# Optimization experiments

Measured on AMD Instinct MI355X. Metric: run time of the kernel, lower is better.

## Reference

```python
import jax, jax.numpy as jnp
import numpy as np

N = 50000          # num nodes
E = 800000         # num edges
DIN = 128          # in_channels
C = 64             # out_channels per head
H = 2              # heads
ED = 32            # edge_dim


def setup_inputs() -> dict:
    key = jax.random.key(0)
    ks = jax.random.split(key, 12)
    s = 1.0 / np.sqrt(DIN)
    se = 1.0 / np.sqrt(ED)
    return {
        "x": jax.random.normal(ks[0], (N, DIN), dtype=jnp.float32),
        "edge_index": jax.random.randint(ks[1], (2, E), 0, N, dtype=jnp.int32),
        "edge_attr": jax.random.normal(ks[2], (E, ED), dtype=jnp.float32),
        "Wq": jax.random.uniform(ks[3], (DIN, H * C), jnp.float32, -s, s),
        "bq": jax.random.uniform(ks[4], (H * C,), jnp.float32, -s, s),
        "Wk": jax.random.uniform(ks[5], (DIN, H * C), jnp.float32, -s, s),
        "bk": jax.random.uniform(ks[6], (H * C,), jnp.float32, -s, s),
        "Wv": jax.random.uniform(ks[7], (DIN, H * C), jnp.float32, -s, s),
        "bv": jax.random.uniform(ks[8], (H * C,), jnp.float32, -s, s),
        "We": jax.random.uniform(ks[9], (ED, H * C), jnp.float32, -se, se),
        "Wskip": jax.random.uniform(ks[10], (DIN, H * C), jnp.float32, -s, s),
        "bskip": jax.random.uniform(ks[11], (H * C,), jnp.float32, -s, s),
    }


def reference(x, edge_index, edge_attr, Wq, bq, Wk, bk, Wv, bv, We, Wskip, bskip):
    src, dst = edge_index[0], edge_index[1]
    # node-level projections [N, H, C]
    q = (x @ Wq + bq).reshape(N, H, C)
    k = (x @ Wk + bk).reshape(N, H, C)
    v = (x @ Wv + bv).reshape(N, H, C)
    e = (edge_attr @ We).reshape(E, H, C)  # lin_edge, no bias

    # per-edge gather
    q_e = q[dst]              # [E, H, C]
    k_e = k[src] + e          # key gets edge features
    alpha = jnp.einsum("ehc,ehc->eh", q_e, k_e) / jnp.sqrt(jnp.float32(C))

    # segment softmax over incoming edges of each dst node
    m = jax.ops.segment_max(alpha, dst, num_segments=N)       # [N, H]
    alpha = jnp.exp(alpha - m[dst])
    denom = jax.ops.segment_sum(alpha, dst, num_segments=N)   # [N, H]
    alpha = alpha / (denom[dst] + 1e-16)

    # weighted aggregation of values (value also gets edge features)
    msg = (v[src] + e) * alpha[..., None]                     # [E, H, C]
    out = jax.ops.segment_sum(msg, dst, num_segments=N)       # [N, H, C]
    out = out.reshape(N, H * C)

    # root weight skip connection (concat=True, beta=False)
    return out + x @ Wskip + bskip
```

## Files before the change

kernel.cpp:

```cpp
#include <hip/hip_runtime.h>
#include <cstdint>

#define NN 50000
#define EE 800000
#define DINC 128
#define HC 128
#define EDC 32
#define CAP 56
#define TILES 1563
#define SCAT_BLKS 3125
#define NB_SCAN 196
#define PREW_GRID (145 + NB_SCAN)

typedef __attribute__((ext_vector_type(8))) short short8;
typedef __attribute__((ext_vector_type(4))) float floatx4;

__device__ __forceinline__ unsigned int pk2(float a, float b){
  unsigned int ua = __float_as_uint(a), ub = __float_as_uint(b);
  ua = (ua + 0x7FFFu + ((ua >> 16) & 1u)) >> 16;
  ub = (ub + 0x7FFFu + ((ub >> 16) & 1u)) & 0xFFFF0000u;
  return ua | ub;
}
__device__ __forceinline__ float bflo(unsigned int p){ return __uint_as_float(p << 16); }
__device__ __forceinline__ float bfhi(unsigned int p){ return __uint_as_float(p & 0xFFFF0000u); }

__device__ __forceinline__ float red32(float r){
  r += __int_as_float(__builtin_amdgcn_update_dpp(0, __float_as_int(r), 0xB1, 0xF, 0xF, true));
  r += __int_as_float(__builtin_amdgcn_update_dpp(0, __float_as_int(r), 0x4E, 0xF, 0xF, true));
  r += __int_as_float(__builtin_amdgcn_update_dpp(0, __float_as_int(r), 0x141, 0xF, 0xF, true));
  r += __int_as_float(__builtin_amdgcn_update_dpp(0, __float_as_int(r), 0x140, 0xF, 0xF, true));
  r += __shfl_xor(r, 16, 32);
  return r;
}

__global__ __launch_bounds__(256) void k_prew(
    const float* __restrict__ Wq, const float* __restrict__ Wk,
    const float* __restrict__ Wv, const float* __restrict__ Wsk,
    const float* __restrict__ We, const float* __restrict__ bq,
    unsigned int* __restrict__ Wp, unsigned int* __restrict__ Wp5,
    float* __restrict__ Pb, int* __restrict__ cnt)
{
  const int b = blockIdx.x, tid = threadIdx.x;
  if (b < 128){
    int idx = b*256 + tid;
    int mat = idx >> 13;
    int r   = idx & 8191;
    int kp  = r >> 7;
    int n   = r & 127;
    const float* W = (mat==0)?Wq:(mat==1)?Wk:(mat==2)?Wv:Wsk;
    Wp[(mat<<13) + n*64 + kp] = pk2(W[(2*kp)*HC + n], W[(2*kp+1)*HC + n]);
  } else if (b < 144){
    if (!Wp5) return;
    int t = (b-128)*256 + tid;
    int kp = t >> 6, n = t & 63;
    int h = n >> 5, j = n & 31;
    const float* wq0 = Wq + (2*kp)*HC + h*64;
    const float* wq1 = wq0 + HC;
    const float* wer = We + j*HC + h*64;
    float d0 = 0.f, d1 = 0.f;
    #pragma unroll 8
    for (int c = 0; c < 64; ++c){
      float w = wer[c];
      d0 += wq0[c]*w; d1 += wq1[c]*w;
    }
    Wp5[n*64 + kp] = pk2(d0, d1);
  } else if (b == 144){
    if (!Wp5 || tid >= 64) return;
    int n = tid, h = n >> 5, j = n & 31;
    const float* wer = We + j*HC + h*64;
    const float* bqh = bq + h*64;
    float s = 0.f;
    #pragma unroll 8
    for (int c = 0; c < 64; ++c) s += bqh[c]*wer[c];
    Pb[n] = s;
  } else {
    int idx = (b-145)*256 + tid;
    if (idx < NN) cnt[idx] = 0;
  }
}

__global__ __launch_bounds__(256) void k_fused(
    const float* __restrict__ x, const unsigned int* __restrict__ Wp,
    const unsigned int* __restrict__ Wp5, const float* __restrict__ Pb,
    const float* __restrict__ bq, const float* __restrict__ bk,
    const float* __restrict__ bv, const float* __restrict__ bsk,
    const int* __restrict__ ei,
    unsigned int* __restrict__ qbf, unsigned int* __restrict__ kvb,
    float* __restrict__ out, float* __restrict__ Pfl,
    int* __restrict__ cnt, int* __restrict__ eidl,
    const int do_scatter)
{
  __shared__ unsigned int sx[32*68];

  if (do_scatter && blockIdx.x >= TILES){
    int e = (blockIdx.x - TILES)*256 + threadIdx.x;
    if (e < EE){
      int d = ei[EE + e];
      int pos = atomicAdd(cnt + d, 1);
      if (pos < CAP) eidl[d*CAP + pos] = e;
    }
    return;
  }

  const int tid = threadIdx.x;
  const int bm  = blockIdx.x * 32;

  for (int idx = tid; idx < 32*32; idx += 256){
    int row = idx >> 5, kq = idx & 31;
    int gr = bm + row;
    unsigned int p0 = 0u, p1 = 0u;
    if (gr < NN){
      float4 v = *(const float4*)(x + (size_t)gr*DINC + 4*kq);
      p0 = pk2(v.x, v.y); p1 = pk2(v.z, v.w);
    }
    sx[row*68 + 2*kq]     = p0;
    sx[row*68 + 2*kq + 1] = p1;
  }
  __syncthreads();

  const int l = tid & 63, wid = tid >> 6;
  const int lm = l & 15, ks = l >> 4;
  const int pe = lm & 1;
  const int n0 = wid * 32;

  short8 a_f[4][2];
  #pragma unroll
  for (int kb = 0; kb < 4; ++kb){
    a_f[kb][0] = *(const short8*)(sx + lm*68      + kb*16 + ks*4);
    a_f[kb][1] = *(const short8*)(sx + (16+lm)*68 + kb*16 + ks*4);
  }

  #pragma unroll
  for (int mat = 0; mat < 4; ++mat){
    const unsigned int* wp = Wp + (mat<<13);
    const float* bi = (mat==0)?bq:(mat==1)?bk:(mat==2)?bv:bsk;

    floatx4 acc[2][2];
    #pragma unroll
    for (int mt=0;mt<2;mt++)
      #pragma unroll
      for (int nt=0;nt<2;nt++) acc[mt][nt] = (floatx4){0.f,0.f,0.f,0.f};

    #pragma unroll
    for (int kb = 0; kb < 4; ++kb){
      short8 b0 = *(const short8*)(wp + (n0+lm)*64    + kb*16 + ks*4);
      short8 b1 = *(const short8*)(wp + (n0+16+lm)*64 + kb*16 + ks*4);
      acc[0][0] = __builtin_amdgcn_mfma_f32_16x16x32_bf16(a_f[kb][0], b0, acc[0][0], 0, 0, 0);
      acc[0][1] = __builtin_amdgcn_mfma_f32_16x16x32_bf16(a_f[kb][0], b1, acc[0][1], 0, 0, 0);
      acc[1][0] = __builtin_amdgcn_mfma_f32_16x16x32_bf16(a_f[kb][1], b0, acc[1][0], 0, 0, 0);
      acc[1][1] = __builtin_amdgcn_mfma_f32_16x16x32_bf16(a_f[kb][1], b1, acc[1][1], 0, 0, 0);
    }

    if (mat < 3){
      #pragma unroll
      for (int nt=0; nt<2; ++nt){
        const int cbase = n0 + nt*16 + (lm & ~1);
        float2 bb = *(const float2*)(bi + cbase);
        const int cp = cbase >> 1;
        #pragma unroll
        for (int mt=0; mt<2; ++mt){
          #pragma unroll
          for (int s=0; s<2; ++s){
            float a_even = acc[mt][nt][2*s];
            float a_odd  = acc[mt][nt][2*s+1];
            float sw_even = __shfl_xor(a_even, 1, 64);
            float sw_odd  = __shfl_xor(a_odd,  1, 64);
            float self = pe ? a_odd  : a_even;
            float part = pe ? sw_odd : sw_even;
            float lo = pe ? part : self;
            float hi = pe ? self : part;
            unsigned int pv = pk2(lo + bb.x, hi + bb.y);
            int gr = bm + mt*16 + ks*4 + 2*s + pe;
            if (gr < NN){
              if (mat == 0)      qbf[gr*64 + cp] = pv;
              else if (mat == 1) kvb[(size_t)gr*128 + cp]      = pv;
              else               kvb[(size_t)gr*128 + 64 + cp] = pv;
            }
          }
        }
      }
    } else {
      #pragma unroll
      for (int nt=0; nt<2; ++nt){
        const int col = n0 + nt*16 + lm;
        float bs = bi[col];
        #pragma unroll
        for (int mt=0; mt<2; ++mt){
          #pragma unroll
          for (int r=0; r<4; ++r){
            int gr = bm + mt*16 + ks*4 + r;
            if (gr < NN) out[(size_t)gr*HC + col] = acc[mt][nt][r] + bs;
          }
        }
      }
    }
  }

  if (Pfl != nullptr && wid < 2){
    floatx4 acc[2][2];
    #pragma unroll
    for (int mt=0;mt<2;mt++)
      #pragma unroll
      for (int nt=0;nt<2;nt++) acc[mt][nt] = (floatx4){0.f,0.f,0.f,0.f};
    #pragma unroll
    for (int kb = 0; kb < 4; ++kb){
      short8 b0 = *(const short8*)(Wp5 + (n0+lm)*64    + kb*16 + ks*4);
      short8 b1 = *(const short8*)(Wp5 + (n0+16+lm)*64 + kb*16 + ks*4);
      acc[0][0] = __builtin_amdgcn_mfma_f32_16x16x32_bf16(a_f[kb][0], b0, acc[0][0], 0, 0, 0);
      acc[0][1] = __builtin_amdgcn_mfma_f32_16x16x32_bf16(a_f[kb][0], b1, acc[0][1], 0, 0, 0);
      acc[1][0] = __builtin_amdgcn_mfma_f32_16x16x32_bf16(a_f[kb][1], b0, acc[1][0], 0, 0, 0);
      acc[1][1] = __builtin_amdgcn_mfma_f32_16x16x32_bf16(a_f[kb][1], b1, acc[1][1], 0, 0, 0);
    }
    #pragma unroll
    for (int nt=0; nt<2; ++nt){
      const int col = n0 + nt*16 + lm;
      float bs = Pb[col];
      #pragma unroll
      for (int mt=0; mt<2; ++mt){
        #pragma unroll
        for (int r=0; r<4; ++r){
          int gr = bm + mt*16 + ks*4 + r;
          if (gr < NN) Pfl[(size_t)gr*64 + col] = acc[mt][nt][r] + bs;
        }
      }
    }
  }
}

__global__ __launch_bounds__(256) void k_count(const int* __restrict__ ei,
    int* __restrict__ cnt)
{
  int e = blockIdx.x*256 + threadIdx.x;
  if (e < EE) atomicAdd(cnt + ei[EE + e], 1);
}
__global__ __launch_bounds__(256) void k_blksum(const int* __restrict__ cnt,
    int* __restrict__ bsum)
{
  __shared__ int s[256];
  int t = threadIdx.x, i = blockIdx.x*256 + t;
  s[t] = (i < NN) ? cnt[i] : 0;
  __syncthreads();
  for (int d = 128; d > 0; d >>= 1){
    if (t < d) s[t] += s[t + d];
    __syncthreads();
  }
  if (t == 0) bsum[blockIdx.x] = s[0];
}
__global__ __launch_bounds__(256) void k_bscan(const int* __restrict__ bsum,
    int* __restrict__ bpre)
{
  __shared__ int s[256];
  int t = threadIdx.x;
  int v = (t < NB_SCAN) ? bsum[t] : 0;
  s[t] = v;
  __syncthreads();
  for (int d = 1; d < 256; d <<= 1){
    int u = (t >= d) ? s[t - d] : 0;
    __syncthreads();
    s[t] += u;
    __syncthreads();
  }
  if (t < NB_SCAN) bpre[t] = s[t] - v;
}
__global__ __launch_bounds__(256) void k_scan3(const int* __restrict__ cnt,
    const int* __restrict__ bpre, int* __restrict__ off, int* __restrict__ woff)
{
  __shared__ int s[256];
  int t = threadIdx.x, i = blockIdx.x*256 + t;
  int v = (i < NN) ? cnt[i] : 0;
  s[t] = v;
  __syncthreads();
  for (int d = 1; d < 256; d <<= 1){
    int u = (t >= d) ? s[t - d] : 0;
    __syncthreads();
    s[t] += u;
    __syncthreads();
  }
  if (i < NN){
    int o = bpre[blockIdx.x] + s[t] - v;
    off[i] = o; woff[i] = o;
  }
}
__global__ __launch_bounds__(256) void k_scatter(const int* __restrict__ ei,
    int* __restrict__ woff, int* __restrict__ eidl)
{
  int e = blockIdx.x*256 + threadIdx.x;
  if (e < EE){
    int d = ei[EE + e];
    int pos = atomicAdd(woff + d, 1);
    eidl[pos] = e;
  }
}

__global__ __launch_bounds__(256) void k_agg(
    const float* __restrict__ eattr, const float* __restrict__ We,
    const unsigned int* __restrict__ qbf, const unsigned int* __restrict__ kvb,
    const int* __restrict__ ei,
    const int* __restrict__ cnt, const int* __restrict__ off,
    const int* __restrict__ eidl, const int fixed, const float* __restrict__ Pfl,
    float* __restrict__ out)
{
  __shared__ float sWeT[128*33];
  __shared__ float sWea[256];
  const int tid = threadIdx.x;
  for (int idx = tid; idx < EDC*HC; idx += 256){
    int jj = idx >> 7, col = idx & 127;
    sWeT[col*33 + jj] = We[idx];
  }
  __syncthreads();

  const int wid = tid >> 6, l = tid & 63;
  const int node = blockIdx.x*4 + wid;
  const int h = l >> 5, j = l & 31;

  int deg = cnt[node]; if (deg > CAP) deg = CAP;
  const size_t beg = fixed ? (size_t)node*CAP : (size_t)off[node];
  int eidL = 0, srcL = 0;
  if (deg > 0){
    eidL = eidl[beg + ((l < deg) ? l : 0)];
    srcL = ei[eidL];
  }
  const unsigned int eaOff = (unsigned int)eidL * (EDC*4);
  const unsigned int kOff  = (unsigned int)srcL * 512u;
  const unsigned int jB = (unsigned int)j * 4u;
  const unsigned int lB = (unsigned int)l * 4u;
  const char* eac = (const char*)eattr;
  const char* kvc = (const char*)kvb;

  const float SC = 0.18033688f;
  unsigned int qp = qbf[node*64 + l];
  float q0 = bflo(qp)*SC, q1 = bfhi(qp)*SC;
  float Pl;
  if (Pfl != nullptr){
    Pl = Pfl[(size_t)node*64 + l] * SC;
  } else {
    const uint4* qrow4 = (const uint4*)(qbf + node*64 + h*32);
    const float* wt = sWeT + (h*64)*33 + j;
    float s = 0.f;
    #pragma unroll
    for (int c4 = 0; c4 < 8; ++c4){
      uint4 u = qrow4[c4];
      int b = 8*c4;
      s += bflo(u.x)*wt[(b+0)*33] + bfhi(u.x)*wt[(b+1)*33];
      s += bflo(u.y)*wt[(b+2)*33] + bfhi(u.y)*wt[(b+3)*33];
      s += bflo(u.z)*wt[(b+4)*33] + bfhi(u.z)*wt[(b+5)*33];
      s += bflo(u.w)*wt[(b+6)*33] + bfhi(u.w)*wt[(b+7)*33];
    }
    Pl = s*SC;
  }

#define GATHER(base, EA, KK, VV)                                 \
  {                                                              \
    _Pragma("unroll")                                            \
    for (int t = 0; t < 4; ++t){                                 \
      int s = (base) + t;                                        \
      int it = (s < deg) ? s : 0;                                \
      unsigned int eo = (unsigned int)__shfl((int)eaOff, it, 64) + jB; \
      unsigned int ko = (unsigned int)__shfl((int)kOff,  it, 64) + lB; \
      EA[t] = *(const float*)(eac + eo);                         \
      KK[t] = *(const unsigned int*)(kvc + ko);                  \
      VV[t] = *(const unsigned int*)(kvc + ko + 256);            \
    }                                                            \
  }

  float acc0=0.f, acc1=0.f, wea=0.f, den=0.f;
  if (deg > 0){
    float eav[4]; unsigned int kk[4], vv[4];
    GATHER(0, eav, kk, vv);

    for (int i = 0; i < deg; i += 4){
      float eavn[4]; unsigned int kkn[4], vvn[4];
      const int inext = i + 4;
      if (inext < deg){
        GATHER(inext, eavn, kkn, vvn);
      }
      float p[4];
      #pragma unroll
      for (int t = 0; t < 4; ++t)
        p[t] = q0*bflo(kk[t]) + q1*bfhi(kk[t]) + Pl*eav[t];
      #pragma unroll
      for (int t = 0; t < 4; ++t) p[t] = red32(p[t]);
      const int nb = deg - i;
      #pragma unroll
      for (int t = 0; t < 4; ++t){
        float a = __builtin_amdgcn_exp2f(p[t]);
        if (t > 0) a = (t < nb) ? a : 0.f;
        den  += a;
        acc0 += a*bflo(vv[t]);
        acc1 += a*bfhi(vv[t]);
        wea  += a*eav[t];
      }
      #pragma unroll
      for (int t = 0; t < 4; ++t){ eav[t] = eavn[t]; kk[t] = kkn[t]; vv[t] = vvn[t]; }
    }
  }
#undef GATHER

  sWea[tid] = wea;
  __syncthreads();
  float rden = 1.0f/(den + 1e-16f);
  float e0 = 0.f, e1 = 0.f;
  const float* w0 = sWeT + (2*l)*33;
  const float* w1 = sWeT + (2*l+1)*33;
  const float* wv = sWea + wid*64 + h*32;
  #pragma unroll
  for (int jj = 0; jj < 32; jj += 4){
    float4 w4 = *(const float4*)(wv + jj);
    e0 += w4.x*w0[jj]; e1 += w4.x*w1[jj];
    e0 += w4.y*w0[jj+1]; e1 += w4.y*w1[jj+1];
    e0 += w4.z*w0[jj+2]; e1 += w4.z*w1[jj+2];
    e0 += w4.w*w0[jj+3]; e1 += w4.w*w1[jj+3];
  }
  float2 sk = *(const float2*)(out + (size_t)node*HC + 2*l);
  float2 o;
  o.x = sk.x + (acc0 + e0)*rden;
  o.y = sk.y + (acc1 + e1)*rden;
  *(float2*)(out + (size_t)node*HC + 2*l) = o;
}

extern "C" void kernel_launch(void* const* d_in, const int* in_sizes, int n_in,
                              void* d_out, int out_size, void* d_ws, size_t ws_size,
                              hipStream_t stream)
{
  const float* x   = (const float*)d_in[0];
  const int*   ei  = (const int*)d_in[1];
  const float* ea  = (const float*)d_in[2];
  const float* Wq  = (const float*)d_in[3];
  const float* bq  = (const float*)d_in[4];
  const float* Wk  = (const float*)d_in[5];
  const float* bk  = (const float*)d_in[6];
  const float* Wv  = (const float*)d_in[7];
  const float* bv  = (const float*)d_in[8];
  const float* We  = (const float*)d_in[9];
  const float* Wsk = (const float*)d_in[10];
  const float* bsk = (const float*)d_in[11];
  float* out = (float*)d_out;

  char* ws = (char*)d_ws;
  unsigned int* qbf = (unsigned int*)(ws);
  unsigned int* kvb = (unsigned int*)(ws + 12800000);
  int* cnt = (int*)(ws + 38400000);

  if (ws_size >= 62800000ull){
    int* eidl = (int*)(ws + 38600000);
    unsigned int* Wp  = (unsigned int*)(ws + 49800064);
    unsigned int* Wp5 = (unsigned int*)(ws + 49931264);
    float* Pb  = (float*)(ws + 49947648);
    float* Pfl = (float*)(ws + 49948160);
    k_prew<<<PREW_GRID, 256, 0, stream>>>(Wq, Wk, Wv, Wsk, We, bq, Wp, Wp5, Pb, cnt);
    k_fused<<<TILES + SCAT_BLKS, 256, 0, stream>>>(
        x, Wp, Wp5, Pb, bq, bk, bv, bsk, ei, qbf, kvb, out, Pfl, cnt, eidl, 1);
    k_agg<<<12500, 256, 0, stream>>>(ea, We, qbf, kvb, ei,
                                     cnt, (const int*)nullptr, eidl, 1, Pfl, out);
  } else if (ws_size >= 50000000ull){
    int* eidl = (int*)(ws + 38600000);
    unsigned int* Wp = (unsigned int*)(ws + 49800064);
    k_prew<<<PREW_GRID, 256, 0, stream>>>(Wq, Wk, Wv, Wsk, We, bq, Wp, nullptr, nullptr, cnt);
    k_fused<<<TILES + SCAT_BLKS, 256, 0, stream>>>(
        x, Wp, nullptr, nullptr, bq, bk, bv, bsk, ei, qbf, kvb, out, nullptr, cnt, eidl, 1);
    k_agg<<<12500, 256, 0, stream>>>(ea, We, qbf, kvb, ei,
                                     cnt, (const int*)nullptr, eidl, 1, nullptr, out);
  } else {
    int* off  = (int*)(ws + 38600000);
    int* woff = (int*)(ws + 38800000);
    int* bsum = (int*)(ws + 39000000);
    int* bpre = (int*)(ws + 39001024);
    int* eidl = (int*)(ws + 39002048);
    unsigned int* Wp = (unsigned int*)(ws + 42202112);
    k_prew<<<PREW_GRID, 256, 0, stream>>>(Wq, Wk, Wv, Wsk, We, bq, Wp, nullptr, nullptr, cnt);
    k_fused<<<TILES, 256, 0, stream>>>(
        x, Wp, nullptr, nullptr, bq, bk, bv, bsk, ei, qbf, kvb, out, nullptr, cnt, nullptr, 0);
    k_count  <<<SCAT_BLKS, 256, 0, stream>>>(ei, cnt);
    k_blksum <<<NB_SCAN, 256, 0, stream>>>(cnt, bsum);
    k_bscan  <<<1, 256, 0, stream>>>(bsum, bpre);
    k_scan3  <<<NB_SCAN, 256, 0, stream>>>(cnt, bpre, off, woff);
    k_scatter<<<SCAT_BLKS, 256, 0, stream>>>(ei, woff, eidl);
    k_agg<<<12500, 256, 0, stream>>>(ea, We, qbf, kvb, ei,
                                     cnt, off, eidl, 0, nullptr, out);
  }
}
```

Measured before the change: 403.1 us.

## Deepen edge gather prefetch to three stages and spread P projection across waves

The aggregation kernel's per-edge gather pipeline now keeps three batches of edge-attribute, key and value loads in flight instead of one. This is meant to hide more global-memory gather latency, at the cost of more registers per thread and possibly lower occupancy. The P projection inside the fused GEMM kernel is split so all four waves each compute one 16-row by 32-column slice, rather than two waves doing all of it. The aggregation kernel is also templated on whether P is precomputed, so that branch is resolved at compile time.

Result: no change. 409.9 us (+1.7%).

```diff
diff --git a/kernel.cpp b/kernel.cpp
--- a/kernel.cpp
+++ b/kernel.cpp
@@ -196,32 +196,27 @@
     }
   }
 
-  if (Pfl != nullptr && wid < 2){
-    floatx4 acc[2][2];
-    #pragma unroll
-    for (int mt=0;mt<2;mt++)
-      #pragma unroll
-      for (int nt=0;nt<2;nt++) acc[mt][nt] = (floatx4){0.f,0.f,0.f,0.f};
+  if (Pfl != nullptr){
+    const int mt = wid >> 1;
+    const int nq = (wid & 1) * 32;
+    floatx4 accp[2];
+    accp[0] = (floatx4){0.f,0.f,0.f,0.f};
+    accp[1] = (floatx4){0.f,0.f,0.f,0.f};
     #pragma unroll
     for (int kb = 0; kb < 4; ++kb){
-      short8 b0 = *(const short8*)(Wp5 + (n0+lm)*64    + kb*16 + ks*4);
-      short8 b1 = *(const short8*)(Wp5 + (n0+16+lm)*64 + kb*16 + ks*4);
-      acc[0][0] = __builtin_amdgcn_mfma_f32_16x16x32_bf16(a_f[kb][0], b0, acc[0][0], 0, 0, 0);
-      acc[0][1] = __builtin_amdgcn_mfma_f32_16x16x32_bf16(a_f[kb][0], b1, acc[0][1], 0, 0, 0);
-      acc[1][0] = __builtin_amdgcn_mfma_f32_16x16x32_bf16(a_f[kb][1], b0, acc[1][0], 0, 0, 0);
-      acc[1][1] = __builtin_amdgcn_mfma_f32_16x16x32_bf16(a_f[kb][1], b1, acc[1][1], 0, 0, 0);
+      short8 b0 = *(const short8*)(Wp5 + (nq+lm)*64    + kb*16 + ks*4);
+      short8 b1 = *(const short8*)(Wp5 + (nq+16+lm)*64 + kb*16 + ks*4);
+      accp[0] = __builtin_amdgcn_mfma_f32_16x16x32_bf16(a_f[kb][mt], b0, accp[0], 0, 0, 0);
+      accp[1] = __builtin_amdgcn_mfma_f32_16x16x32_bf16(a_f[kb][mt], b1, accp[1], 0, 0, 0);
     }
     #pragma unroll
     for (int nt=0; nt<2; ++nt){
-      const int col = n0 + nt*16 + lm;
+      const int col = nq + nt*16 + lm;
       float bs = Pb[col];
       #pragma unroll
-      for (int mt=0; mt<2; ++mt){
-        #pragma unroll
-        for (int r=0; r<4; ++r){
-          int gr = bm + mt*16 + ks*4 + r;
-          if (gr < NN) Pfl[(size_t)gr*64 + col] = acc[mt][nt][r] + bs;
-        }
+      for (int r=0; r<4; ++r){
+        int gr = bm + mt*16 + ks*4 + r;
+        if (gr < NN) Pfl[(size_t)gr*64 + col] = accp[nt][r] + bs;
       }
     }
   }
@@ -292,6 +287,7 @@
   }
 }
 
+template<int HASP>
 __global__ __launch_bounds__(256) void k_agg(
     const float* __restrict__ eattr, const float* __restrict__ We,
     const unsigned int* __restrict__ qbf, const unsigned int* __restrict__ kvb,
@@ -331,7 +327,7 @@
   unsigned int qp = qbf[node*64 + l];
   float q0 = bflo(qp)*SC, q1 = bfhi(qp)*SC;
   float Pl;
-  if (Pfl != nullptr){
+  if (HASP){
     Pl = Pfl[(size_t)node*64 + l] * SC;
   } else {
     const uint4* qrow4 = (const uint4*)(qbf + node*64 + h*32);
@@ -365,19 +361,21 @@
 
   float acc0=0.f, acc1=0.f, wea=0.f, den=0.f;
   if (deg > 0){
-    float eav[4]; unsigned int kk[4], vv[4];
-    GATHER(0, eav, kk, vv);
+    float ea0[4], ea1[4], ea2[4];
+    unsigned int kk0[4], kk1[4], kk2[4], vv0[4], vv1[4], vv2[4];
+    GATHER(0, ea0, kk0, vv0);
+    GATHER(4, ea1, kk1, vv1);
+    GATHER(8, ea2, kk2, vv2);
 
     for (int i = 0; i < deg; i += 4){
-      float eavn[4]; unsigned int kkn[4], vvn[4];
-      const int inext = i + 4;
-      if (inext < deg){
-        GATHER(inext, eavn, kkn, vvn);
+      float ean[4]; unsigned int kkn[4], vvn[4];
+      if (i + 12 < deg){
+        GATHER(i+12, ean, kkn, vvn);
       }
       float p[4];
       #pragma unroll
       for (int t = 0; t < 4; ++t)
-        p[t] = q0*bflo(kk[t]) + q1*bfhi(kk[t]) + Pl*eav[t];
+        p[t] = q0*bflo(kk0[t]) + q1*bfhi(kk0[t]) + Pl*ea0[t];
       #pragma unroll
       for (int t = 0; t < 4; ++t) p[t] = red32(p[t]);
       const int nb = deg - i;
@@ -386,12 +384,16 @@
         float a = __builtin_amdgcn_exp2f(p[t]);
         if (t > 0) a = (t < nb) ? a : 0.f;
         den  += a;
-        acc0 += a*bflo(vv[t]);
-        acc1 += a*bfhi(vv[t]);
-        wea  += a*eav[t];
-      }
-      #pragma unroll
-      for (int t = 0; t < 4; ++t){ eav[t] = eavn[t]; kk[t] = kkn[t]; vv[t] = vvn[t]; }
+        acc0 += a*bflo(vv0[t]);
+        acc1 += a*bfhi(vv0[t]);
+        wea  += a*ea0[t];
+      }
+      #pragma unroll
+      for (int t = 0; t < 4; ++t){
+        ea0[t] = ea1[t]; kk0[t] = kk1[t]; vv0[t] = vv1[t];
+        ea1[t] = ea2[t]; kk1[t] = kk2[t]; vv1[t] = vv2[t];
+        ea2[t] = ean[t]; kk2[t] = kkn[t]; vv2[t] = vvn[t];
+      }
     }
   }
 #undef GATHER
@@ -450,16 +452,16 @@
     k_prew<<<PREW_GRID, 256, 0, stream>>>(Wq, Wk, Wv, Wsk, We, bq, Wp, Wp5, Pb, cnt);
     k_fused<<<TILES + SCAT_BLKS, 256, 0, stream>>>(
         x, Wp, Wp5, Pb, bq, bk, bv, bsk, ei, qbf, kvb, out, Pfl, cnt, eidl, 1);
-    k_agg<<<12500, 256, 0, stream>>>(ea, We, qbf, kvb, ei,
-                                     cnt, (const int*)nullptr, eidl, 1, Pfl, out);
+    k_agg<1><<<12500, 256, 0, stream>>>(ea, We, qbf, kvb, ei,
+                                        cnt, (const int*)nullptr, eidl, 1, Pfl, out);
   } else if (ws_size >= 50000000ull){
     int* eidl = (int*)(ws + 38600000);
     unsigned int* Wp = (unsigned int*)(ws + 49800064);
     k_prew<<<PREW_GRID, 256, 0, stream>>>(Wq, Wk, Wv, Wsk, We, bq, Wp, nullptr, nullptr, cnt);
     k_fused<<<TILES + SCAT_BLKS, 256, 0, stream>>>(
         x, Wp, nullptr, nullptr, bq, bk, bv, bsk, ei, qbf, kvb, out, nullptr, cnt, eidl, 1);
-    k_agg<<<12500, 256, 0, stream>>>(ea, We, qbf, kvb, ei,
-                                     cnt, (const int*)nullptr, eidl, 1, nullptr, out);
+    k_agg<0><<<12500, 256, 0, stream>>>(ea, We, qbf, kvb, ei,
+                                        cnt, (const int*)nullptr, eidl, 1, nullptr, out);
   } else {
     int* off  = (int*)(ws + 38600000);
     int* woff = (int*)(ws + 38800000);
@@ -475,7 +477,7 @@
     k_bscan  <<<1, 256, 0, stream>>>(bsum, bpre);
     k_scan3  <<<NB_SCAN, 256, 0, stream>>>(cnt, bpre, off, woff);
     k_scatter<<<SCAT_BLKS, 256, 0, stream>>>(ei, woff, eidl);
-    k_agg<<<12500, 256, 0, stream>>>(ea, We, qbf, kvb, ei,
-                                     cnt, off, eidl, 0, nullptr, out);
-  }
-}
+    k_agg<0><<<12500, 256, 0, stream>>>(ea, We, qbf, kvb, ei,
+                                        cnt, off, eidl, 0, nullptr, out);
+  }
+}
```
